# Performance work log

Hardware: AMD Instinct MI355X
Metric: run time of the kernel (lower is better)

Reference implementation:

```python
import jax, jax.numpy as jnp
import numpy as np

N = 131072      # octree nodes at this depth
C_IN = 256      # in_channels == out_channels
C_B = 64        # bottleneck channels = out_channels // 4
K = 27          # 3x3x3 octree kernel neighborhood
EPS = 1e-5


def _bn(x, g, b, m, v):
    # inference-style BatchNorm with given running stats
    return (x - m) * (g * jax.lax.rsqrt(v + EPS)) + b


def setup_inputs() -> dict:
    key = jax.random.key(0)
    ks = jax.random.split(key, 20)
    inp = {
        "data": jax.random.normal(ks[0], (N, C_IN), dtype=jnp.float32),
        "neigh": jax.random.randint(ks[1], (N, K), 0, N, dtype=jnp.int32),
        "depth": 6,
        # conv1x1a (Linear, no bias) + BN
        "w1": jax.random.normal(ks[2], (C_IN, C_B), dtype=jnp.float32) * 0.05,
        "bn1_g": jax.random.uniform(ks[3], (C_B,), dtype=jnp.float32) + 0.5,
        "bn1_b": jax.random.normal(ks[4], (C_B,), dtype=jnp.float32) * 0.1,
        "bn1_m": jax.random.normal(ks[5], (C_B,), dtype=jnp.float32) * 0.1,
        "bn1_v": jax.random.uniform(ks[6], (C_B,), dtype=jnp.float32) + 0.5,
        # octree conv3x3 (27-neighbor gather + GEMM, no bias) + BN
        "w3": jax.random.normal(ks[7], (K, C_B, C_B), dtype=jnp.float32) * 0.02,
        "bn2_g": jax.random.uniform(ks[8], (C_B,), dtype=jnp.float32) + 0.5,
        "bn2_b": jax.random.normal(ks[9], (C_B,), dtype=jnp.float32) * 0.1,
        "bn2_m": jax.random.normal(ks[10], (C_B,), dtype=jnp.float32) * 0.1,
        "bn2_v": jax.random.uniform(ks[11], (C_B,), dtype=jnp.float32) + 0.5,
        # conv1x1b + BN (no ReLU)
        "w2": jax.random.normal(ks[12], (C_B, C_IN), dtype=jnp.float32) * 0.05,
        "bn3_g": jax.random.uniform(ks[13], (C_IN,), dtype=jnp.float32) + 0.5,
        "bn3_b": jax.random.normal(ks[14], (C_IN,), dtype=jnp.float32) * 0.1,
        "bn3_m": jax.random.normal(ks[15], (C_IN,), dtype=jnp.float32) * 0.1,
        "bn3_v": jax.random.uniform(ks[16], (C_IN,), dtype=jnp.float32) + 0.5,
    }
    return inp


def reference(data, neigh, depth, w1, bn1_g, bn1_b, bn1_m, bn1_v,
              w3, bn2_g, bn2_b, bn2_m, bn2_v,
              w2, bn3_g, bn3_b, bn3_m, bn3_v):
    # conv1x1a + BN + ReLU
    c1 = jax.nn.relu(_bn(data @ w1, bn1_g, bn1_b, bn1_m, bn1_v))  # [N, C_B]
    # octree conv3x3: gather 27 neighbors then contract with [K, C_B, C_B]
    gathered = c1[neigh]                                          # [N, K, C_B]
    c2 = jnp.einsum('nkc,kcd->nd', gathered, w3)                  # [N, C_B]
    c2 = jax.nn.relu(_bn(c2, bn2_g, bn2_b, bn2_m, bn2_v))
    # conv1x1b + BN (no relu)
    c3 = _bn(c2 @ w2, bn3_g, bn3_b, bn3_m, bn3_v)                 # [N, C_IN]
    # residual (in_channels == out_channels -> identity shortcut) + ReLU
    return jax.nn.relu(c3 + data)
```

## Files before the change

### kernel.cpp

```cpp
#include <hip/hip_runtime.h>

#define CIN 256
#define CB 64
#define KNB 27

typedef __attribute__((ext_vector_type(8))) short short8_t;
typedef __attribute__((ext_vector_type(4))) float f32x4;
typedef __attribute__((ext_vector_type(4))) int   i32x4;

__device__ inline unsigned short f2bf(float f) {
    union { float f; unsigned u; } x; x.f = f;
    unsigned r = x.u + 0x7fffu + ((x.u >> 16) & 1u);
    return (unsigned short)(r >> 16);
}
__device__ inline float bf2f(unsigned short h) {
    union { unsigned u; float f; } x; x.u = ((unsigned)h) << 16; return x.f;
}
__device__ inline f32x4 mfma16(short8_t a, short8_t b, f32x4 c) {
    return __builtin_amdgcn_mfma_f32_16x16x32_bf16(a, b, c, 0, 0, 0);
}
__device__ inline i32x4 mfma_i8(i32x4 a, i32x4 b, i32x4 c) {
    return __builtin_amdgcn_mfma_i32_16x16x64_i8(a, b, c, 0, 0, 0);
}

__global__ __launch_bounds__(256) void prep_a_kernel(
    const float* __restrict__ w1, const float* __restrict__ w2,
    const float* __restrict__ g1, const float* __restrict__ b1, const float* __restrict__ m1, const float* __restrict__ v1,
    const float* __restrict__ g2, const float* __restrict__ b2, const float* __restrict__ m2, const float* __restrict__ v2,
    const float* __restrict__ g3, const float* __restrict__ b3, const float* __restrict__ m3, const float* __restrict__ v3,
    unsigned short* __restrict__ w1p, unsigned short* __restrict__ w2p,
    float* __restrict__ bias1, float* __restrict__ bias2, float* __restrict__ bias3)
{
    int t = blockIdx.x * 256 + threadIdx.x;
    if (t < 16384) {
        int j = t & 7, lane = (t >> 3) & 63, tt = (t >> 9) & 3, s = t >> 11;
        int c = s * 32 + (lane >> 4) * 8 + j;
        int d = tt * 16 + (lane & 15);
        float sc = g1[d] * rsqrtf(v1[d] + 1e-5f);
        w1p[t] = f2bf(w1[c * CB + d] * sc);
    } else if (t < 32768) {
        int u = t - 16384;
        int j = u & 7, lane = (u >> 3) & 63, mt = (u >> 9) & 15, s = u >> 13;
        int c = s * 32 + (lane >> 4) * 8 + j;
        int d = mt * 16 + (lane & 15);
        float sc = g3[d] * rsqrtf(v3[d] + 1e-5f);
        w2p[u] = f2bf(w2[c * CIN + d] * sc);
    } else if (t < 33152) {
        int u = t - 32768;
        if (u < 64)       { float sc = g1[u] * rsqrtf(v1[u] + 1e-5f); bias1[u] = b1[u] - m1[u] * sc; }
        else if (u < 128) { int d = u - 64;  float sc = g2[d] * rsqrtf(v2[d] + 1e-5f); bias2[d] = b2[d] - m2[d] * sc; }
        else              { int d = u - 128; float sc = g3[d] * rsqrtf(v3[d] + 1e-5f); bias3[d] = b3[d] - m3[d] * sc; }
    }
}

__global__ __launch_bounds__(256) void prep_bq_kernel(
    const float* __restrict__ w3, const float* __restrict__ g2, const float* __restrict__ v2,
    signed char* __restrict__ w3q, unsigned* __restrict__ amax)
{
    __shared__ float sc2[64];
    __shared__ float sm[4];
    int tid = threadIdx.x;
    if (tid < 64) sc2[tid] = g2[tid] * rsqrtf(v2[tid] + 1e-5f);
    __syncthreads();

    const float4* w34 = (const float4*)w3;
    float m = 0.f;
    for (int e = tid; e < KNB * CB * CB / 4; e += 256) {
        float4 v = w34[e];
        int d0 = (e * 4) & 63;
        m = fmaxf(m, fabsf(v.x * sc2[d0]));
        m = fmaxf(m, fabsf(v.y * sc2[d0 + 1]));
        m = fmaxf(m, fabsf(v.z * sc2[d0 + 2]));
        m = fmaxf(m, fabsf(v.w * sc2[d0 + 3]));
    }
#pragma unroll
    for (int off = 32; off; off >>= 1) m = fmaxf(m, __shfl_xor(m, off));
    if ((tid & 63) == 0) sm[tid >> 6] = m;
    __syncthreads();
    float mm = fmaxf(fmaxf(sm[0], sm[1]), fmaxf(sm[2], sm[3]));
    float inv = mm > 0.f ? 127.f / mm : 0.f;

    int u = blockIdx.x * 256 + tid;
    int j = u & 15, lane = (u >> 4) & 63, tile = (u >> 10) & 3, k = u >> 12;
    int c = (lane >> 4) * 16 + j;
    int d = tile * 16 + (lane & 15);
    int q = __float2int_rn(w3[(k * CB + c) * CB + d] * sc2[d] * inv);
    q = q > 127 ? 127 : (q < -127 ? -127 : q);
    w3q[u] = (signed char)q;
    if (blockIdx.x == 0 && tid == 0) amax[1] = __float_as_uint(mm);
}

__global__ __launch_bounds__(256) void k1_conv1x1a(
    const float* __restrict__ data, const unsigned short* __restrict__ w1p,
    const float* __restrict__ bias1, unsigned short* __restrict__ c1b,
    float* __restrict__ blockmax)
{
    __shared__ short8_t w1s[2048];
    __shared__ float smax[4];
    int tid = threadIdx.x;
    const short8_t* wsrc = (const short8_t*)w1p;
#pragma unroll
    for (int i = 0; i < 8; i++) w1s[tid + i * 256] = wsrc[tid + i * 256];

    int lane = tid & 63, wave = tid >> 6;
    int g = lane >> 4, r = lane & 15;
    int rowbase = blockIdx.x * 128 + wave * 32;
    f32x4 acc[2][4] = {};
    __syncthreads();

#pragma unroll
    for (int s = 0; s < 8; s++) {
        short8_t a[2];
#pragma unroll
        for (int sub = 0; sub < 2; sub++) {
            const float* ap = data + (size_t)(rowbase + sub * 16 + r) * CIN + s * 32 + g * 8;
            float4 f0 = *(const float4*)ap;
            float4 f1 = *(const float4*)(ap + 4);
            short8_t av;
            av[0] = (short)f2bf(f0.x); av[1] = (short)f2bf(f0.y);
            av[2] = (short)f2bf(f0.z); av[3] = (short)f2bf(f0.w);
            av[4] = (short)f2bf(f1.x); av[5] = (short)f2bf(f1.y);
            av[6] = (short)f2bf(f1.z); av[7] = (short)f2bf(f1.w);
            a[sub] = av;
        }
#pragma unroll
        for (int t = 0; t < 4; t++) {
            short8_t b = w1s[(s * 4 + t) * 64 + lane];
            acc[0][t] = mfma16(a[0], b, acc[0][t]);
            acc[1][t] = mfma16(a[1], b, acc[1][t]);
        }
    }

    float mloc = 0.f;
#pragma unroll
    for (int sub = 0; sub < 2; sub++)
#pragma unroll
        for (int t = 0; t < 4; t++) {
            int col = t * 16 + r;
            float bs = bias1[col];
#pragma unroll
            for (int i = 0; i < 4; i++) {
                int row = rowbase + sub * 16 + g * 4 + i;
                float v = fmaxf(acc[sub][t][i] + bs, 0.f);
                mloc = fmaxf(mloc, v);
                c1b[row * CB + col] = f2bf(v);
            }
        }
#pragma unroll
    for (int off = 32; off; off >>= 1) mloc = fmaxf(mloc, __shfl_xor(mloc, off));
    if (lane == 0) smax[wave] = mloc;
    __syncthreads();
    if (tid == 0)
        blockmax[blockIdx.x] = fmaxf(fmaxf(smax[0], smax[1]), fmaxf(smax[2], smax[3]));
}

__global__ __launch_bounds__(256) void quant_c1_kernel(
    const unsigned short* __restrict__ c1b, const float* __restrict__ blockmax,
    signed char* __restrict__ c1q, unsigned* __restrict__ amax)
{
    __shared__ float sm[4];
    int tid = threadIdx.x;
    float4 bm = ((const float4*)blockmax)[tid];
    float m = fmaxf(fmaxf(bm.x, bm.y), fmaxf(bm.z, bm.w));
#pragma unroll
    for (int off = 32; off; off >>= 1) m = fmaxf(m, __shfl_xor(m, off));
    if ((tid & 63) == 0) sm[tid >> 6] = m;
    __syncthreads();
    float s1 = fmaxf(fmaxf(sm[0], sm[1]), fmaxf(sm[2], sm[3]));
    float inv = s1 > 0.f ? 127.f / s1 : 0.f;

    int t = blockIdx.x * 256 + tid;
    const short8_t* src = (const short8_t*)c1b;
    short8_t v0 = src[t * 2], v1 = src[t * 2 + 1];
    int ow[4];
#pragma unroll
    for (int h = 0; h < 4; h++) {
        int w = 0;
#pragma unroll
        for (int e = 0; e < 4; e++) {
            unsigned short hv = (unsigned short)((h < 2 ? v0 : v1)[(h & 1) * 4 + e]);
            int q = __float2int_rn(bf2f(hv) * inv);
            q = q > 127 ? 127 : q;
            w |= (q & 0xff) << (e * 8);
        }
        ow[h] = w;
    }
    ((int4*)c1q)[t] = make_int4(ow[0], ow[1], ow[2], ow[3]);
    if (blockIdx.x == 0 && tid == 0) amax[0] = __float_as_uint(s1);
}

__global__ __launch_bounds__(64, 3) void k23_fused(
    const signed char* __restrict__ c1q, const int* __restrict__ neigh,
    const signed char* __restrict__ w3q, const float* __restrict__ bias2,
    const unsigned* __restrict__ amax,
    const unsigned short* __restrict__ w2p, const float* __restrict__ bias3,
    const float* __restrict__ data, float* __restrict__ out)
{
    __shared__ int nidx[32 * KNB];
    __shared__ unsigned short cst[32 * 68];
    int tid = threadIdx.x;
    int rowbase = blockIdx.x * 32;

    const int4* nsrc = (const int4*)(neigh + (size_t)rowbase * KNB);
#pragma unroll
    for (int i = 0; i < 4; i++) {
        int p = tid + i * 64;
        if (p < 216) ((int4*)nidx)[p] = nsrc[p];
    }

    int g = tid >> 4, r = tid & 15;
    float sf = __uint_as_float(amax[0]) * __uint_as_float(amax[1]) * (1.f / (127.f * 127.f));
    __syncthreads();

    const i32x4* bq = (const i32x4*)w3q;
    i32x4 iacc[2][4] = {};
#pragma unroll
    for (int k = 0; k < KNB; k++) {
        i32x4 b0 = bq[k * 256 + tid];
        i32x4 b1 = bq[k * 256 + 64 + tid];
        i32x4 b2 = bq[k * 256 + 128 + tid];
        i32x4 b3 = bq[k * 256 + 192 + tid];
        int i0 = nidx[r * KNB + k];
        int i1 = nidx[(16 + r) * KNB + k];
        i32x4 a0 = *(const i32x4*)(c1q + (size_t)i0 * CB + g * 16);
        i32x4 a1 = *(const i32x4*)(c1q + (size_t)i1 * CB + g * 16);
        iacc[0][0] = mfma_i8(a0, b0, iacc[0][0]);
        iacc[1][0] = mfma_i8(a1, b0, iacc[1][0]);
        iacc[0][1] = mfma_i8(a0, b1, iacc[0][1]);
        iacc[1][1] = mfma_i8(a1, b1, iacc[1][1]);
        iacc[0][2] = mfma_i8(a0, b2, iacc[0][2]);
        iacc[1][2] = mfma_i8(a1, b2, iacc[1][2]);
        iacc[0][3] = mfma_i8(a0, b3, iacc[0][3]);
        iacc[1][3] = mfma_i8(a1, b3, iacc[1][3]);
    }

#pragma unroll
    for (int sub = 0; sub < 2; sub++)
#pragma unroll
        for (int t = 0; t < 4; t++) {
            int col = t * 16 + r;
            float bs = bias2[col];
#pragma unroll
            for (int i = 0; i < 4; i++) {
                int lrow = sub * 16 + g * 4 + i;
                cst[lrow * 68 + col] = f2bf(fmaxf((float)iacc[sub][t][i] * sf + bs, 0.f));
            }
        }
    __syncthreads();

    short8_t bfr[2][2];
#pragma unroll
    for (int sub = 0; sub < 2; sub++)
#pragma unroll
        for (int s = 0; s < 2; s++)
            bfr[sub][s] = *(const short8_t*)&cst[(sub * 16 + r) * 68 + s * 32 + g * 8];

    const short8_t* abase = (const short8_t*)w2p;
#pragma unroll
    for (int h = 0; h < 2; h++) {
        f32x4 acc2[2][8] = {};
#pragma unroll
        for (int mt = 0; mt < 8; mt++) {
            short8_t a0 = abase[(h * 8 + mt) * 64 + tid];
            short8_t a1 = abase[(16 + h * 8 + mt) * 64 + tid];
            acc2[0][mt] = mfma16(a0, bfr[0][0], acc2[0][mt]);
            acc2[0][mt] = mfma16(a1, bfr[0][1], acc2[0][mt]);
            acc2[1][mt] = mfma16(a0, bfr[1][0], acc2[1][mt]);
            acc2[1][mt] = mfma16(a1, bfr[1][1], acc2[1][mt]);
        }
#pragma unroll
        for (int sub = 0; sub < 2; sub++)
#pragma unroll
            for (int mt = 0; mt < 8; mt++) {
                int col0 = (h * 8 + mt) * 16 + g * 4;
                int rowg = rowbase + sub * 16 + r;
                float4 bs = *(const float4*)(bias3 + col0);
                float4 dv = *(const float4*)(data + (size_t)rowg * CIN + col0);
                f32x4 v = acc2[sub][mt];
                float4 res;
                res.x = fmaxf(v[0] + bs.x + dv.x, 0.f);
                res.y = fmaxf(v[1] + bs.y + dv.y, 0.f);
                res.z = fmaxf(v[2] + bs.z + dv.z, 0.f);
                res.w = fmaxf(v[3] + bs.w + dv.w, 0.f);
                *(float4*)(out + (size_t)rowg * CIN + col0) = res;
            }
    }
}

extern "C" void kernel_launch(void* const* d_in, const int* in_sizes, int n_in,
                              void* d_out, int out_size, void* d_ws, size_t ws_size,
                              hipStream_t stream)
{
    const float* data = (const float*)d_in[0];
    const int* neigh  = (const int*)d_in[1];
    const float* w1 = (const float*)d_in[3];
    const float* g1 = (const float*)d_in[4];
    const float* b1 = (const float*)d_in[5];
    const float* m1 = (const float*)d_in[6];
    const float* v1 = (const float*)d_in[7];
    const float* w3 = (const float*)d_in[8];
    const float* g2 = (const float*)d_in[9];
    const float* b2 = (const float*)d_in[10];
    const float* m2 = (const float*)d_in[11];
    const float* v2 = (const float*)d_in[12];
    const float* w2 = (const float*)d_in[13];
    const float* g3 = (const float*)d_in[14];
    const float* b3 = (const float*)d_in[15];
    const float* m3 = (const float*)d_in[16];
    const float* v3 = (const float*)d_in[17];
    float* out = (float*)d_out;

    char* ws = (char*)d_ws;
    unsigned short* c1b = (unsigned short*)ws;
    signed char*    c1q = (signed char*)(ws + 16777216);
    unsigned short* w1p = (unsigned short*)(ws + 25165824);
    signed char*    w3q = (signed char*)(ws + 25198592);
    unsigned short* w2p = (unsigned short*)(ws + 25309184);
    float* bias1 = (float*)(ws + 25341952);
    float* bias2 = bias1 + 64;
    float* bias3 = bias1 + 128;
    unsigned* amax = (unsigned*)(ws + 25343488);
    float* blockmax = (float*)(ws + 25343552);

    int n = in_sizes[0] / CIN;

    hipLaunchKernelGGL(prep_a_kernel, dim3(130), dim3(256), 0, stream,
                       w1, w2, g1, b1, m1, v1, g2, b2, m2, v2, g3, b3, m3, v3,
                       w1p, w2p, bias1, bias2, bias3);
    hipLaunchKernelGGL(prep_bq_kernel, dim3(432), dim3(256), 0, stream,
                       w3, g2, v2, w3q, amax);
    hipLaunchKernelGGL(k1_conv1x1a, dim3(n / 128), dim3(256), 0, stream,
                       data, w1p, bias1, c1b, blockmax);
    hipLaunchKernelGGL(quant_c1_kernel, dim3(2048), dim3(256), 0, stream,
                       c1b, blockmax, c1q, amax);
    hipLaunchKernelGGL(k23_fused, dim3(n / 32), dim3(64), 0, stream,
                       c1q, neigh, w3q, bias2, amax, w2p, bias3, data, out);
}
```

Before: 186.9 us.

## Split fused conv3x3+conv1x1b kernel into two kernels via bf16 intermediate

```diff
diff --git a/kernel.cpp b/kernel.cpp
--- a/kernel.cpp
+++ b/kernel.cpp
@@ -189,39 +189,39 @@
     if (blockIdx.x == 0 && tid == 0) amax[0] = __float_as_uint(s1);
 }
 
-__global__ __launch_bounds__(64, 3) void k23_fused(
+__global__ __launch_bounds__(128, 6) void k2_conv3x3(
     const signed char* __restrict__ c1q, const int* __restrict__ neigh,
     const signed char* __restrict__ w3q, const float* __restrict__ bias2,
-    const unsigned* __restrict__ amax,
-    const unsigned short* __restrict__ w2p, const float* __restrict__ bias3,
-    const float* __restrict__ data, float* __restrict__ out)
-{
-    __shared__ int nidx[32 * KNB];
-    __shared__ unsigned short cst[32 * 68];
-    int tid = threadIdx.x;
-    int rowbase = blockIdx.x * 32;
+    const unsigned* __restrict__ amax, unsigned short* __restrict__ c2b)
+{
+    __shared__ int nidx[64 * KNB];
+    int tid = threadIdx.x;
+    int rowbase = blockIdx.x * 64;
 
     const int4* nsrc = (const int4*)(neigh + (size_t)rowbase * KNB);
 #pragma unroll
     for (int i = 0; i < 4; i++) {
-        int p = tid + i * 64;
-        if (p < 216) ((int4*)nidx)[p] = nsrc[p];
-    }
-
-    int g = tid >> 4, r = tid & 15;
+        int p = tid + i * 128;
+        if (p < 432) ((int4*)nidx)[p] = nsrc[p];
+    }
+
+    int lane = tid & 63, wave = tid >> 6;
+    int g = lane >> 4, r = lane & 15;
+    int lr0 = wave * 32 + r, lr1 = wave * 32 + 16 + r;
     float sf = __uint_as_float(amax[0]) * __uint_as_float(amax[1]) * (1.f / (127.f * 127.f));
     __syncthreads();
 
     const i32x4* bq = (const i32x4*)w3q;
     i32x4 iacc[2][4] = {};
+
 #pragma unroll
     for (int k = 0; k < KNB; k++) {
-        i32x4 b0 = bq[k * 256 + tid];
-        i32x4 b1 = bq[k * 256 + 64 + tid];
-        i32x4 b2 = bq[k * 256 + 128 + tid];
-        i32x4 b3 = bq[k * 256 + 192 + tid];
-        int i0 = nidx[r * KNB + k];
-        int i1 = nidx[(16 + r) * KNB + k];
+        i32x4 b0 = bq[k * 256 + lane];
+        i32x4 b1 = bq[k * 256 + 64 + lane];
+        i32x4 b2 = bq[k * 256 + 128 + lane];
+        i32x4 b3 = bq[k * 256 + 192 + lane];
+        int i0 = nidx[lr0 * KNB + k];
+        int i1 = nidx[lr1 * KNB + k];
         i32x4 a0 = *(const i32x4*)(c1q + (size_t)i0 * CB + g * 16);
         i32x4 a1 = *(const i32x4*)(c1q + (size_t)i1 * CB + g * 16);
         iacc[0][0] = mfma_i8(a0, b0, iacc[0][0]);
@@ -242,49 +242,58 @@
             float bs = bias2[col];
 #pragma unroll
             for (int i = 0; i < 4; i++) {
-                int lrow = sub * 16 + g * 4 + i;
-                cst[lrow * 68 + col] = f2bf(fmaxf((float)iacc[sub][t][i] * sf + bs, 0.f));
+                int row = rowbase + wave * 32 + sub * 16 + g * 4 + i;
+                float v = fmaxf((float)iacc[sub][t][i] * sf + bs, 0.f);
+                c2b[row * CB + col] = f2bf(v);
             }
         }
-    __syncthreads();
-
-    short8_t bfr[2][2];
-#pragma unroll
-    for (int sub = 0; sub < 2; sub++)
+}
+
+__global__ __launch_bounds__(256) void k3_conv1x1b(
+    const unsigned short* __restrict__ c2b, const unsigned short* __restrict__ w2p,
+    const float* __restrict__ bias3, const float* __restrict__ data,
+    float* __restrict__ out)
+{
+    int tid = threadIdx.x;
+    int lane = tid & 63, wave = tid >> 6;
+    int g = lane >> 4, r = lane & 15;
+    int rowbase = blockIdx.x * 64;
+
+    const short8_t* abase = (const short8_t*)w2p;
+    short8_t bfr[4][2];
+#pragma unroll
+    for (int sub = 0; sub < 4; sub++)
 #pragma unroll
         for (int s = 0; s < 2; s++)
-            bfr[sub][s] = *(const short8_t*)&cst[(sub * 16 + r) * 68 + s * 32 + g * 8];
-
-    const short8_t* abase = (const short8_t*)w2p;
-#pragma unroll
-    for (int h = 0; h < 2; h++) {
-        f32x4 acc2[2][8] = {};
-#pragma unroll
-        for (int mt = 0; mt < 8; mt++) {
-            short8_t a0 = abase[(h * 8 + mt) * 64 + tid];
-            short8_t a1 = abase[(16 + h * 8 + mt) * 64 + tid];
-            acc2[0][mt] = mfma16(a0, bfr[0][0], acc2[0][mt]);
-            acc2[0][mt] = mfma16(a1, bfr[0][1], acc2[0][mt]);
-            acc2[1][mt] = mfma16(a0, bfr[1][0], acc2[1][mt]);
-            acc2[1][mt] = mfma16(a1, bfr[1][1], acc2[1][mt]);
-        }
-#pragma unroll
-        for (int sub = 0; sub < 2; sub++)
-#pragma unroll
-            for (int mt = 0; mt < 8; mt++) {
-                int col0 = (h * 8 + mt) * 16 + g * 4;
-                int rowg = rowbase + sub * 16 + r;
-                float4 bs = *(const float4*)(bias3 + col0);
-                float4 dv = *(const float4*)(data + (size_t)rowg * CIN + col0);
-                f32x4 v = acc2[sub][mt];
-                float4 res;
-                res.x = fmaxf(v[0] + bs.x + dv.x, 0.f);
-                res.y = fmaxf(v[1] + bs.y + dv.y, 0.f);
-                res.z = fmaxf(v[2] + bs.z + dv.z, 0.f);
-                res.w = fmaxf(v[3] + bs.w + dv.w, 0.f);
-                *(float4*)(out + (size_t)rowg * CIN + col0) = res;
-            }
-    }
+            bfr[sub][s] = *(const short8_t*)(c2b + (size_t)(rowbase + sub * 16 + r) * CB + s * 32 + g * 8);
+
+    f32x4 acc2[4][4] = {};
+#pragma unroll
+    for (int s = 0; s < 2; s++)
+#pragma unroll
+        for (int mt = 0; mt < 4; mt++) {
+            short8_t a = abase[(s * 16 + wave * 4 + mt) * 64 + lane];
+#pragma unroll
+            for (int sub = 0; sub < 4; sub++)
+                acc2[sub][mt] = mfma16(a, bfr[sub][s], acc2[sub][mt]);
+        }
+
+#pragma unroll
+    for (int sub = 0; sub < 4; sub++)
+#pragma unroll
+        for (int mt = 0; mt < 4; mt++) {
+            int col0 = (wave * 4 + mt) * 16 + g * 4;
+            int rowg = rowbase + sub * 16 + r;
+            float4 bs = *(const float4*)(bias3 + col0);
+            float4 dv = *(const float4*)(data + (size_t)rowg * CIN + col0);
+            f32x4 v = acc2[sub][mt];
+            float4 res;
+            res.x = fmaxf(v[0] + bs.x + dv.x, 0.f);
+            res.y = fmaxf(v[1] + bs.y + dv.y, 0.f);
+            res.z = fmaxf(v[2] + bs.z + dv.z, 0.f);
+            res.w = fmaxf(v[3] + bs.w + dv.w, 0.f);
+            *(float4*)(out + (size_t)rowg * CIN + col0) = res;
+        }
 }
 
 extern "C" void kernel_launch(void* const* d_in, const int* in_sizes, int n_in,
@@ -312,6 +321,7 @@
 
     char* ws = (char*)d_ws;
     unsigned short* c1b = (unsigned short*)ws;
+    unsigned short* c2b = (unsigned short*)ws;
     signed char*    c1q = (signed char*)(ws + 16777216);
     unsigned short* w1p = (unsigned short*)(ws + 25165824);
     signed char*    w3q = (signed char*)(ws + 25198592);
@@ -333,6 +343,8 @@
                        data, w1p, bias1, c1b, blockmax);
     hipLaunchKernelGGL(quant_c1_kernel, dim3(2048), dim3(256), 0, stream,
                        c1b, blockmax, c1q, amax);
-    hipLaunchKernelGGL(k23_fused, dim3(n / 32), dim3(64), 0, stream,
-                       c1q, neigh, w3q, bias2, amax, w2p, bias3, data, out);
-}
+    hipLaunchKernelGGL(k2_conv3x3, dim3(n / 64), dim3(128), 0, stream,
+                       c1q, neigh, w3q, bias2, amax, c2b);
+    hipLaunchKernelGGL(k3_conv1x1b, dim3(n / 64), dim3(256), 0, stream,
+                       c2b, w2p, bias3, data, out);
+}
```

New measurement: 207.7 us. +11.1%, slower.
